# Kernel optimization log

Measured on AMD Instinct MI355X. Metric: run time of the kernel, lower is better.

The kernel has to match this reference:

```python
import jax, jax.numpy as jnp
from jax import lax
import numpy as np

N_BATCH = 1024
FEATURE_NUM = 128
NUM_CLASSES = 1000
MAX_MODES = 10
TEMPERATURE = 1.0
NU = FEATURE_NUM // 2 - 1  # p/2 - 1 = 63


def log_ive_pair(x):
    """Vectorized Miller downward recurrence, done in log domain for stability
    (equivalent to the torch code's dynamic rescaling-by-log trick).
    Returns (log Ive_NU(x), log Ive_{NU+1}(x)) elementwise over x."""
    logx = jnp.log(x)
    z = jnp.zeros_like(x)
    init = (z, jnp.full_like(x, -jnp.inf), z, z)  # logI_{2nu}=0, logI_{2nu+1}=-inf
    i_vals = jnp.arange(2 * NU, 0, -1)

    def step(carry, i):
        logI, logI1, s0, s1 = carry
        fi = i.astype(logx.dtype)
        # I_{i-1} = (2 i / x) I_i + I_{i+1}  ->  logaddexp in log domain
        new_logI = jnp.logaddexp(jnp.log(2.0 * fi) - logx + logI, logI1)
        # after the update, old logI is log I_i; record at i==NU and i==NU+1
        s0 = jnp.where(i == NU, logI, s0)
        s1 = jnp.where(i == NU + 1, logI, s1)
        return (new_logI, logI, s0, s1), None

    (logI0, _, s0, s1), _ = lax.scan(step, init, i_vals)
    log_ive0 = jnp.log(jax.scipy.special.i0e(x))
    return log_ive0 + s0 - logI0, log_ive0 + s1 - logI0


@jax.custom_vjp
def log_ratio_c(k, logc):
    lognu, _ = log_ive_pair(k)
    return lognu + k - NU * jnp.log(k + 1e-20) - logc


def _lrc_fwd(k, logc):
    lognu, lognu1 = log_ive_pair(k)
    out = lognu + k - NU * jnp.log(k + 1e-20) - logc
    # custom backward of LogRatioC: grad wrt k = min(I_{nu+1}/I_nu, 1); None wrt logc
    return out, (jnp.minimum(jnp.exp(lognu1 - lognu), 1.0), jnp.zeros_like(logc))


def _lrc_bwd(res, g):
    ratio, zlogc = res
    return (ratio * g, zlogc)


log_ratio_c.defvjp(_lrc_fwd, _lrc_bwd)


def _forward(features, Ave_old, Amount_old, labels):
    # --- soft_assign_mode on detached features vs. old prototypes ---
    f_d = lax.stop_gradient(features)
    ave_sel = Ave_old[labels]  # [N, M, D] gather by label
    num = jnp.einsum('nd,nmd->nm', f_d, ave_sel)
    den = jnp.maximum(jnp.linalg.norm(f_d, axis=1, keepdims=True)
                      * jnp.linalg.norm(ave_sel, axis=2), 1e-8)
    soft = jax.nn.softmax(num / den / TEMPERATURE, axis=1)  # [N, M]
    # --- update_CV (estimator_old): label-indexed scatter of soft assignments ---
    sum_oh = jax.ops.segment_sum(soft, labels, num_segments=NUM_CLASSES)  # [C, M]
    wfeat = jax.ops.segment_sum(soft[:, :, None] * f_d[:, None, :], labels,
                                num_segments=NUM_CLASSES)  # [C, M, D]
    ave_cma = wfeat / jnp.where(sum_oh == 0, 1.0, sum_oh)[:, :, None]
    w = sum_oh / (sum_oh + Amount_old)
    w = jnp.where(jnp.isnan(w), 0.0, w)
    Ave = lax.stop_gradient(Ave_old * (1.0 - w[:, :, None]) + ave_cma * w[:, :, None])
    # --- update_kappa: vMF concentration + Bessel recurrence for log normalizer ---
    R = jnp.linalg.norm(Ave, axis=2)  # [C, M]
    kappa = FEATURE_NUM * R / (1.0 - R * R)
    kappa = jnp.where((kappa > 1e5) | (kappa < 0), 1e5, kappa)
    lognu, _ = log_ive_pair(kappa)
    logc = lognu + kappa - NU * jnp.log(kappa + 1e-20)
    # --- contrastive logits ---
    Ave_n = Ave / jnp.maximum(jnp.linalg.norm(Ave, axis=2, keepdims=True), 1e-12)
    sims = features @ Ave_n.reshape(NUM_CLASSES * MAX_MODES, FEATURE_NUM).T / TEMPERATURE
    kf = kappa.reshape(-1)  # [C*M]
    kappa_new = jnp.sqrt(kf * kf + 2.0 * kf * sims + 1.0)  # [N, C*M]
    logits = log_ratio_c(kappa_new, logc.reshape(-1))
    return jnp.max(logits.reshape(-1, NUM_CLASSES, MAX_MODES), axis=2)  # [N, C]


def setup_inputs() -> dict:
    key = jax.random.key(0)
    k1, k2, k3 = jax.random.split(key, 3)
    features = jax.random.normal(k1, (N_BATCH, FEATURE_NUM), dtype=jnp.float32)
    features = features / jnp.linalg.norm(features, axis=1, keepdims=True)
    Ave_old = jax.random.normal(k2, (NUM_CLASSES, MAX_MODES, FEATURE_NUM), dtype=jnp.float32)
    Ave_old = 0.9 * Ave_old / jnp.linalg.norm(Ave_old, axis=2, keepdims=True)  # R<1 so kappa>0
    Amount_old = 100.0 * jnp.ones((NUM_CLASSES, MAX_MODES), dtype=jnp.float32)
    labels = jax.random.randint(k3, (N_BATCH,), 0, NUM_CLASSES, dtype=jnp.int32)
    return {"features": features, "Ave_old": Ave_old, "Amount_old": Amount_old, "labels": labels}


def reference(features, Ave_old, Amount_old, labels):
    return _forward(features, Ave_old, Amount_old, labels)
```

## Files before the change

### kernel.cpp

```cpp
#include <hip/hip_runtime.h>
#include <math.h>

#define C_NUM 1000
#define M_MODES 10
#define CMTOT (C_NUM * M_MODES)
#define D_FEAT 128
#define N_BATCH 1024

typedef _Float16 h16;
typedef h16 h16x2 __attribute__((ext_vector_type(2)));
typedef h16 half8 __attribute__((ext_vector_type(8)));
typedef float f32x4 __attribute__((ext_vector_type(4)));

#define OFF_FEATH  0
#define OFF_AVEH   65536
#define OFF_CMC    705536

__global__ __launch_bounds__(256) void k2_fused(
    const float* __restrict__ feat,
    const float* __restrict__ ave_old,
    const float* __restrict__ amount,
    const int*   __restrict__ labels,
    h16*   __restrict__ feat_h,
    h16*   __restrict__ ave_h,
    float* __restrict__ cmc)
{
    const int c    = blockIdx.x;
    const int tid  = threadIdx.x;
    const int wave = tid >> 6;
    const int lane = tid & 63;

    __shared__ int   s_cnt;
    __shared__ int   s_list[N_BATCH];
    __shared__ float s_an[M_MODES];
    __shared__ float s_soft[N_BATCH * 10 / 4];

    const float2* feat2 = (const float2*)feat;
    const float2* ave2  = (const float2*)ave_old;

    if (c < 256) {
        const int n = c * 4 + wave;
        float2 f = feat2[n * 64 + lane];
        ((h16x2*)(feat_h + n * D_FEAT))[lane] = (h16x2){(h16)f.x, (h16)f.y};
    }

    if (tid == 0) s_cnt = 0;
    __syncthreads();

    for (int n = tid; n < N_BATCH; n += 256)
        if (labels[n] == c) { int p = atomicAdd(&s_cnt, 1); s_list[p] = n; }

    #pragma unroll
    for (int m = wave; m < M_MODES; m += 4) {
        float2 a = ave2[(c * M_MODES + m) * 64 + lane];
        float an = a.x * a.x + a.y * a.y;
        #pragma unroll
        for (int s = 1; s < 64; s <<= 1) an += __shfl_xor(an, s);
        if (lane == 0) s_an[m] = sqrtf(an);
    }
    __syncthreads();

    const int nc = s_cnt < 256 ? s_cnt : 256;

    for (int i = wave; i < nc; i += 4) {
        const int n = s_list[i];
        float2 f = feat2[n * 64 + lane];
        float fn = f.x * f.x + f.y * f.y;
        float d[M_MODES];
        #pragma unroll
        for (int m = 0; m < M_MODES; ++m) {
            float2 a = ave2[(c * M_MODES + m) * 64 + lane];
            d[m] = f.x * a.x + f.y * a.y;
        }
        #pragma unroll
        for (int s = 1; s < 64; s <<= 1) {
            fn += __shfl_xor(fn, s);
            #pragma unroll
            for (int m = 0; m < M_MODES; ++m) d[m] += __shfl_xor(d[m], s);
        }
        const float fnorm = sqrtf(fn);
        float sc[M_MODES], mx = -INFINITY;
        #pragma unroll
        for (int m = 0; m < M_MODES; ++m) {
            float den = fmaxf(fnorm * s_an[m], 1e-8f);
            sc[m] = d[m] / den;
            mx = fmaxf(mx, sc[m]);
        }
        float se = 0.f;
        #pragma unroll
        for (int m = 0; m < M_MODES; ++m) { sc[m] = __expf(sc[m] - mx); se += sc[m]; }
        const float inv = 1.0f / se;
        if (lane == 0) {
            #pragma unroll
            for (int m = 0; m < M_MODES; ++m) s_soft[i * M_MODES + m] = sc[m] * inv;
        }
    }
    __syncthreads();

    for (int m = wave; m < M_MODES; m += 4) {
        const int wid = c * M_MODES + m;
        float ssum = 0.f, wx = 0.f, wy = 0.f;
        for (int i = 0; i < nc; ++i) {
            float s  = s_soft[i * M_MODES + m];
            float2 f = feat2[s_list[i] * 64 + lane];
            ssum += s;
            wx = fmaf(s, f.x, wx);
            wy = fmaf(s, f.y, wy);
        }
        const float am = amount[wid];
        float w = ssum / (ssum + am);
        if (!(w == w)) w = 0.0f;
        const float dn = (ssum == 0.0f) ? 1.0f : ssum;

        float2 ao = ave2[wid * 64 + lane];
        float ax = ao.x * (1.0f - w) + (wx / dn) * w;
        float ay = ao.y * (1.0f - w) + (wy / dn) * w;

        float r2 = ax * ax + ay * ay;
        #pragma unroll
        for (int s2 = 1; s2 < 64; s2 <<= 1) r2 += __shfl_xor(r2, s2);
        const float R = sqrtf(r2);

        float kappa = 128.0f * R / (1.0f - R * R);
        if (kappa > 1e5f || kappa < 0.0f) kappa = 1e5f;

        const float nrm = fmaxf(R, 1e-12f);
        ((h16x2*)(ave_h + wid * D_FEAT))[lane] = (h16x2){(h16)(ax / nrm), (h16)(ay / nrm)};

        if (lane == 0) {
            float k   = kappa;
            float swk = sqrtf(fmaf(k, k, 3969.0f));
            float i1  = 1.0f / (63.0f + swk);
            float i2  = 1.0f / swk;
            float c1  = 1.0f - 63.0f * i1 - 0.5f * i2;
            float c2  = 31.5f * i1 * i1 + 0.25f * i2 * i2;
            float c3  = -(21.0f * i1 * i1 * i1 + (1.0f / 6.0f) * i2 * i2 * i2);
            float4* p = (float4*)(cmc + wid * 8);
            p[0] = make_float4(2.0f * k, fmaf(k, k, 3970.0f), swk, c1);
            p[1] = make_float4(c2, c3, 0.0f, 0.0f);
        }
    }
}

#define SWZ(row, j) (((row) << 8) + ((((j) ^ ((row) & 15))) << 4))
#define LSTR 81
__global__ __launch_bounds__(512) void k3_logits(
    const h16*   __restrict__ feat_h,
    const h16*   __restrict__ ave_h,
    const float* __restrict__ cmc,
    float* __restrict__ out)
{
    __shared__ __align__(16) char smem[128 * 256 + 80 * 256];
    char*  smemB = smem + 128 * 256;
    float* ls    = (float*)smem;

    const int tid    = threadIdx.x;
    const int cmbase = blockIdx.x * 80;
    const int nbase  = blockIdx.y * 128;

    {
        const float4* src = (const float4*)(feat_h + nbase * D_FEAT);
        #pragma unroll
        for (int i = 0; i < 4; ++i) {
            int e = tid + i * 512;
            int r = e >> 4, j = e & 15;
            *(float4*)(smem + SWZ(r, j)) = src[e];
        }
    }
    for (int e = tid; e < 1280; e += 512) {
        int r = e >> 4, j = e & 15;
        *(float4*)(smemB + SWZ(r, j)) = ((const float4*)(ave_h + cmbase * D_FEAT))[e];
    }
    __syncthreads();

    const int wave = tid >> 6;
    const int lane = tid & 63;
    const int lrow = lane & 15;
    const int lhi  = lane >> 4;

    f32x4 acc[5] = {};
    #pragma unroll
    for (int ks = 0; ks < 4; ++ks) {
        half8 a = *(const half8*)(smem + SWZ(wave * 16 + lrow, ks * 4 + lhi));
        #pragma unroll
        for (int t = 0; t < 5; ++t) {
            half8 b = *(const half8*)(smemB + SWZ(t * 16 + lrow, ks * 4 + lhi));
            acc[t] = __builtin_amdgcn_mfma_f32_16x16x32_f16(a, b, acc[t], 0, 0, 0);
        }
    }

    #pragma unroll
    for (int t = 0; t < 5; ++t) {
        const int cm = cmbase + t * 16 + lrow;
        float4 p0 = ((const float4*)(cmc + cm * 8))[0];
        float4 p1 = ((const float4*)(cmc + cm * 8))[1];
        #pragma unroll
        for (int r = 0; r < 4; ++r) {
            float s   = acc[t][r];
            float swn = sqrtf(fmaf(p0.x, s, p0.y));
            float num = fmaf(p0.x, s, 1.0f);
            float D   = __fdividef(num, swn + p0.z);
            acc[t][r] = D * fmaf(D, fmaf(D, p1.y, p1.x), p0.w);
        }
    }

    __syncthreads();
    #pragma unroll
    for (int t = 0; t < 5; ++t)
        #pragma unroll
        for (int r = 0; r < 4; ++r)
            ls[(wave * 16 + lhi * 4 + r) * LSTR + t * 16 + lrow] = acc[t][r];
    __syncthreads();

    #pragma unroll
    for (int rep = 0; rep < 2; ++rep) {
        int id = rep * 512 + tid;
        int q  = id >> 3;
        int cl = id & 7;
        const float* row = ls + q * LSTR + cl * 10;
        float mx = row[0];
        #pragma unroll
        for (int j = 1; j < 10; ++j) mx = fmaxf(mx, row[j]);
        out[(nbase + q) * C_NUM + blockIdx.x * 8 + cl] = mx;
    }
}

extern "C" void kernel_launch(void* const* d_in, const int* in_sizes, int n_in,
                              void* d_out, int out_size, void* d_ws, size_t ws_size,
                              hipStream_t stream) {
    const float* feat    = (const float*)d_in[0];
    const float* ave_old = (const float*)d_in[1];
    const float* amount  = (const float*)d_in[2];
    const int*   labels  = (const int*)d_in[3];
    float* out = (float*)d_out;
    float* ws  = (float*)d_ws;

    h16*   feat_h = (h16*)(ws + OFF_FEATH);
    h16*   ave_h  = (h16*)(ws + OFF_AVEH);
    float* cmc    = ws + OFF_CMC;

    k2_fused<<<dim3(C_NUM), dim3(256), 0, stream>>>(
        feat, ave_old, amount, labels, feat_h, ave_h, cmc);

    k3_logits<<<dim3(125, 8), dim3(512), 0, stream>>>(
        feat_h, ave_h, cmc, out);
}
```

Baseline: 90.02 us.

## Split prep kernel to one wave per class-mode with ballot-based label scan

The per-class prep kernel is restructured so each wave owns one (class, mode) pair across 2500 blocks, plus 256 blocks for the feature fp16 conversion. The shared-memory label list, atomics and block barriers are replaced by a wave-level ballot over labels. Each wave recomputes the soft assignment for its matching samples redundantly, which removes the intra-block syncs and raises parallelism. The cost is redundant softmax work per mode and every wave reading all labels.

```diff
diff --git a/kernel.cpp b/kernel.cpp
--- a/kernel.cpp
+++ b/kernel.cpp
@@ -16,7 +16,7 @@
 #define OFF_AVEH   65536
 #define OFF_CMC    705536
 
-__global__ __launch_bounds__(256) void k2_fused(
+__global__ __launch_bounds__(256) void prep(
     const float* __restrict__ feat,
     const float* __restrict__ ave_old,
     const float* __restrict__ amount,
@@ -25,120 +25,109 @@
     h16*   __restrict__ ave_h,
     float* __restrict__ cmc)
 {
-    const int c    = blockIdx.x;
-    const int tid  = threadIdx.x;
-    const int wave = tid >> 6;
-    const int lane = tid & 63;
-
-    __shared__ int   s_cnt;
-    __shared__ int   s_list[N_BATCH];
-    __shared__ float s_an[M_MODES];
-    __shared__ float s_soft[N_BATCH * 10 / 4];
-
+    const int wave = threadIdx.x >> 6;
+    const int lane = threadIdx.x & 63;
     const float2* feat2 = (const float2*)feat;
     const float2* ave2  = (const float2*)ave_old;
 
-    if (c < 256) {
-        const int n = c * 4 + wave;
+    if (blockIdx.x >= 2500) {
+        const int n = (blockIdx.x - 2500) * 4 + wave;
         float2 f = feat2[n * 64 + lane];
         ((h16x2*)(feat_h + n * D_FEAT))[lane] = (h16x2){(h16)f.x, (h16)f.y};
-    }
-
-    if (tid == 0) s_cnt = 0;
-    __syncthreads();
-
-    for (int n = tid; n < N_BATCH; n += 256)
-        if (labels[n] == c) { int p = atomicAdd(&s_cnt, 1); s_list[p] = n; }
-
-    #pragma unroll
-    for (int m = wave; m < M_MODES; m += 4) {
-        float2 a = ave2[(c * M_MODES + m) * 64 + lane];
-        float an = a.x * a.x + a.y * a.y;
-        #pragma unroll
-        for (int s = 1; s < 64; s <<= 1) an += __shfl_xor(an, s);
-        if (lane == 0) s_an[m] = sqrtf(an);
-    }
-    __syncthreads();
-
-    const int nc = s_cnt < 256 ? s_cnt : 256;
-
-    for (int i = wave; i < nc; i += 4) {
-        const int n = s_list[i];
-        float2 f = feat2[n * 64 + lane];
-        float fn = f.x * f.x + f.y * f.y;
-        float d[M_MODES];
-        #pragma unroll
-        for (int m = 0; m < M_MODES; ++m) {
-            float2 a = ave2[(c * M_MODES + m) * 64 + lane];
-            d[m] = f.x * a.x + f.y * a.y;
-        }
-        #pragma unroll
-        for (int s = 1; s < 64; s <<= 1) {
-            fn += __shfl_xor(fn, s);
-            #pragma unroll
-            for (int m = 0; m < M_MODES; ++m) d[m] += __shfl_xor(d[m], s);
-        }
-        const float fnorm = sqrtf(fn);
-        float sc[M_MODES], mx = -INFINITY;
-        #pragma unroll
-        for (int m = 0; m < M_MODES; ++m) {
-            float den = fmaxf(fnorm * s_an[m], 1e-8f);
-            sc[m] = d[m] / den;
-            mx = fmaxf(mx, sc[m]);
-        }
-        float se = 0.f;
-        #pragma unroll
-        for (int m = 0; m < M_MODES; ++m) { sc[m] = __expf(sc[m] - mx); se += sc[m]; }
-        const float inv = 1.0f / se;
-        if (lane == 0) {
-            #pragma unroll
-            for (int m = 0; m < M_MODES; ++m) s_soft[i * M_MODES + m] = sc[m] * inv;
-        }
-    }
-    __syncthreads();
-
-    for (int m = wave; m < M_MODES; m += 4) {
-        const int wid = c * M_MODES + m;
-        float ssum = 0.f, wx = 0.f, wy = 0.f;
-        for (int i = 0; i < nc; ++i) {
-            float s  = s_soft[i * M_MODES + m];
-            float2 f = feat2[s_list[i] * 64 + lane];
-            ssum += s;
-            wx = fmaf(s, f.x, wx);
-            wy = fmaf(s, f.y, wy);
-        }
-        const float am = amount[wid];
-        float w = ssum / (ssum + am);
-        if (!(w == w)) w = 0.0f;
-        const float dn = (ssum == 0.0f) ? 1.0f : ssum;
-
-        float2 ao = ave2[wid * 64 + lane];
-        float ax = ao.x * (1.0f - w) + (wx / dn) * w;
-        float ay = ao.y * (1.0f - w) + (wy / dn) * w;
-
-        float r2 = ax * ax + ay * ay;
-        #pragma unroll
-        for (int s2 = 1; s2 < 64; s2 <<= 1) r2 += __shfl_xor(r2, s2);
-        const float R = sqrtf(r2);
-
-        float kappa = 128.0f * R / (1.0f - R * R);
-        if (kappa > 1e5f || kappa < 0.0f) kappa = 1e5f;
-
-        const float nrm = fmaxf(R, 1e-12f);
-        ((h16x2*)(ave_h + wid * D_FEAT))[lane] = (h16x2){(h16)(ax / nrm), (h16)(ay / nrm)};
-
-        if (lane == 0) {
-            float k   = kappa;
-            float swk = sqrtf(fmaf(k, k, 3969.0f));
-            float i1  = 1.0f / (63.0f + swk);
-            float i2  = 1.0f / swk;
-            float c1  = 1.0f - 63.0f * i1 - 0.5f * i2;
-            float c2  = 31.5f * i1 * i1 + 0.25f * i2 * i2;
-            float c3  = -(21.0f * i1 * i1 * i1 + (1.0f / 6.0f) * i2 * i2 * i2);
-            float4* p = (float4*)(cmc + wid * 8);
-            p[0] = make_float4(2.0f * k, fmaf(k, k, 3970.0f), swk, c1);
-            p[1] = make_float4(c2, c3, 0.0f, 0.0f);
-        }
+        return;
+    }
+
+    const int cm = blockIdx.x * 4 + wave;
+    const int c  = cm / M_MODES;
+    const int m  = cm - c * M_MODES;
+
+    float2 ao[M_MODES];
+    #pragma unroll
+    for (int j = 0; j < M_MODES; ++j) ao[j] = ave2[(c * M_MODES + j) * 64 + lane];
+
+    float an[M_MODES];
+    #pragma unroll
+    for (int j = 0; j < M_MODES; ++j) an[j] = ao[j].x * ao[j].x + ao[j].y * ao[j].y;
+    #pragma unroll
+    for (int s = 1; s < 64; s <<= 1)
+        #pragma unroll
+        for (int j = 0; j < M_MODES; ++j) an[j] += __shfl_xor(an[j], s);
+    #pragma unroll
+    for (int j = 0; j < M_MODES; ++j) an[j] = sqrtf(an[j]);
+
+    float ssum = 0.f, wx = 0.f, wy = 0.f;
+    const int4* lab4 = (const int4*)labels;
+    #pragma unroll
+    for (int k4 = 0; k4 < 4; ++k4) {
+        int4 lv = lab4[lane + k4 * 64];
+        #pragma unroll
+        for (int j = 0; j < 4; ++j) {
+            int lbl = (j == 0) ? lv.x : (j == 1) ? lv.y : (j == 2) ? lv.z : lv.w;
+            unsigned long long mask = __ballot(lbl == c);
+            while (mask) {
+                int lz = __ffsll((long long)mask) - 1;
+                mask &= mask - 1;
+                const int n = 4 * lz + 256 * k4 + j;
+                float2 f = feat2[n * 64 + lane];
+                float d[M_MODES], fn = f.x * f.x + f.y * f.y;
+                #pragma unroll
+                for (int t = 0; t < M_MODES; ++t)
+                    d[t] = f.x * ao[t].x + f.y * ao[t].y;
+                #pragma unroll
+                for (int s = 1; s < 64; s <<= 1) {
+                    fn += __shfl_xor(fn, s);
+                    #pragma unroll
+                    for (int t = 0; t < M_MODES; ++t) d[t] += __shfl_xor(d[t], s);
+                }
+                const float fnorm = sqrtf(fn);
+                float sc[M_MODES], mx = -INFINITY;
+                #pragma unroll
+                for (int t = 0; t < M_MODES; ++t) {
+                    float den = fmaxf(fnorm * an[t], 1e-8f);
+                    sc[t] = d[t] / den;
+                    mx = fmaxf(mx, sc[t]);
+                }
+                float se = 0.f;
+                #pragma unroll
+                for (int t = 0; t < M_MODES; ++t) { sc[t] = __expf(sc[t] - mx); se += sc[t]; }
+                const float soft_m = sc[m] / se;
+                ssum += soft_m;
+                wx = fmaf(soft_m, f.x, wx);
+                wy = fmaf(soft_m, f.y, wy);
+            }
+        }
+    }
+
+    const float am = amount[cm];
+    float w = ssum / (ssum + am);
+    if (!(w == w)) w = 0.0f;
+    const float dn = (ssum == 0.0f) ? 1.0f : ssum;
+
+    float ax = ao[m].x * (1.0f - w) + (wx / dn) * w;
+    float ay = ao[m].y * (1.0f - w) + (wy / dn) * w;
+
+    float r2 = ax * ax + ay * ay;
+    #pragma unroll
+    for (int s = 1; s < 64; s <<= 1) r2 += __shfl_xor(r2, s);
+    const float R = sqrtf(r2);
+
+    float kappa = 128.0f * R / (1.0f - R * R);
+    if (kappa > 1e5f || kappa < 0.0f) kappa = 1e5f;
+
+    const float nrm = fmaxf(R, 1e-12f);
+    ((h16x2*)(ave_h + cm * D_FEAT))[lane] = (h16x2){(h16)(ax / nrm), (h16)(ay / nrm)};
+
+    if (lane == 0) {
+        float k   = kappa;
+        float swk = sqrtf(fmaf(k, k, 3969.0f));
+        float i1  = 1.0f / (63.0f + swk);
+        float i2  = 1.0f / swk;
+        float c1  = 1.0f - 63.0f * i1 - 0.5f * i2;
+        float c2  = 31.5f * i1 * i1 + 0.25f * i2 * i2;
+        float c3  = -(21.0f * i1 * i1 * i1 + (1.0f / 6.0f) * i2 * i2 * i2);
+        float4* p = (float4*)(cmc + cm * 8);
+        p[0] = make_float4(2.0f * k, fmaf(k, k, 3970.0f), swk, c1);
+        p[1] = make_float4(c2, c3, 0.0f, 0.0f);
     }
 }
 
@@ -239,7 +228,7 @@
     h16*   ave_h  = (h16*)(ws + OFF_AVEH);
     float* cmc    = ws + OFF_CMC;
 
-    k2_fused<<<dim3(C_NUM), dim3(256), 0, stream>>>(
+    prep<<<dim3(2756), dim3(256), 0, stream>>>(
         feat, ave_old, amount, labels, feat_h, ave_h, cmc);
 
     k3_logits<<<dim3(125, 8), dim3(512), 0, stream>>>(
```

New measurement: 115.3 us. 1.28x slower.

## Permute prototype rows in LDS so mode max reduces in registers

Applied to the files above, without the earlier changes.

Prototype rows are reordered as they are loaded into shared memory so that each lane's MFMA output columns belong to a single class, with its modes spread across tiles and a lane pair. The per-class max over modes is then taken in registers plus one shuffle, and results are written straight to global memory. This removes the shared-memory staging of logits, two barriers and the strided LDS reduction pass. In exchange, output stores are narrower (8 lanes per row) and the loader does an integer divide per row.

```diff
diff --git a/kernel.cpp b/kernel.cpp
--- a/kernel.cpp
+++ b/kernel.cpp
@@ -143,7 +143,6 @@
 }
 
 #define SWZ(row, j) (((row) << 8) + ((((j) ^ ((row) & 15))) << 4))
-#define LSTR 81
 __global__ __launch_bounds__(512) void k3_logits(
     const h16*   __restrict__ feat_h,
     const h16*   __restrict__ ave_h,
@@ -151,8 +150,7 @@
     float* __restrict__ out)
 {
     __shared__ __align__(16) char smem[128 * 256 + 80 * 256];
-    char*  smemB = smem + 128 * 256;
-    float* ls    = (float*)smem;
+    char* smemB = smem + 128 * 256;
 
     const int tid    = threadIdx.x;
     const int cmbase = blockIdx.x * 80;
@@ -169,7 +167,10 @@
     }
     for (int e = tid; e < 1280; e += 512) {
         int r = e >> 4, j = e & 15;
-        *(float4*)(smemB + SWZ(r, j)) = ((const float4*)(ave_h + cmbase * D_FEAT))[e];
+        int cl = r / 10;
+        int m  = r - cl * 10;
+        int p  = ((m >> 1) << 4) + ((m & 1) << 3) + cl;
+        *(float4*)(smemB + SWZ(p, j)) = ((const float4*)(ave_h + cmbase * D_FEAT))[e];
     }
     __syncthreads();
 
@@ -189,39 +190,29 @@
         }
     }
 
+    float mx[4] = { -INFINITY, -INFINITY, -INFINITY, -INFINITY };
     #pragma unroll
     for (int t = 0; t < 5; ++t) {
-        const int cm = cmbase + t * 16 + lrow;
+        const int cm = (cmbase + (lrow & 7) * 10) + 2 * t + (lrow >> 3);
         float4 p0 = ((const float4*)(cmc + cm * 8))[0];
         float4 p1 = ((const float4*)(cmc + cm * 8))[1];
         #pragma unroll
         for (int r = 0; r < 4; ++r) {
             float s   = acc[t][r];
             float swn = sqrtf(fmaf(p0.x, s, p0.y));
-            float num = fmaf(p0.x, s, 1.0f);
-            float D   = __fdividef(num, swn + p0.z);
-            acc[t][r] = D * fmaf(D, fmaf(D, p1.y, p1.x), p0.w);
-        }
-    }
-
-    __syncthreads();
-    #pragma unroll
-    for (int t = 0; t < 5; ++t)
+            float D   = __fdividef(fmaf(p0.x, s, 1.0f), swn + p0.z);
+            float lg  = D * fmaf(D, fmaf(D, p1.y, p1.x), p0.w);
+            mx[r] = fmaxf(mx[r], lg);
+        }
+    }
+    #pragma unroll
+    for (int r = 0; r < 4; ++r) mx[r] = fmaxf(mx[r], __shfl_xor(mx[r], 8));
+
+    if (lrow < 8) {
         #pragma unroll
         for (int r = 0; r < 4; ++r)
-            ls[(wave * 16 + lhi * 4 + r) * LSTR + t * 16 + lrow] = acc[t][r];
-    __syncthreads();
-
-    #pragma unroll
-    for (int rep = 0; rep < 2; ++rep) {
-        int id = rep * 512 + tid;
-        int q  = id >> 3;
-        int cl = id & 7;
-        const float* row = ls + q * LSTR + cl * 10;
-        float mx = row[0];
-        #pragma unroll
-        for (int j = 1; j < 10; ++j) mx = fmaxf(mx, row[j]);
-        out[(nbase + q) * C_NUM + blockIdx.x * 8 + cl] = mx;
+            out[(nbase + wave * 16 + lhi * 4 + r) * C_NUM
+                + blockIdx.x * 8 + lrow] = mx[r];
     }
 }
 
```

Result: no change. 90.92 us (+1.0%).
